# Optimization experiments

Hardware: AMD Instinct MI355X
Metric: run time of the kernel (lower is better)

The kernel has to match this reference:

```python
import jax, jax.numpy as jnp
import numpy as np

N_NODES = 100000
N_EDGES = 1600000
D_IN = 256
D_OUT = 128


def setup_inputs() -> dict:
    key = jax.random.key(0)
    k1, k2, k3, k4, k5, k6 = jax.random.split(key, 6)
    inp = {
        "input": jax.random.normal(k1, (N_NODES, D_IN), dtype=jnp.float32),
        "edge_row": jax.random.randint(k2, (N_EDGES,), 0, N_NODES),
        "edge_col": jax.random.randint(k3, (N_EDGES,), 0, N_NODES),
        "edge_val": jax.random.uniform(k4, (N_EDGES,), dtype=jnp.float32),
        "W": jax.random.normal(k5, (D_IN, D_OUT), dtype=jnp.float32) * (1.0 / np.sqrt(D_IN)),
        "b": jax.random.normal(k6, (D_OUT,), dtype=jnp.float32) * 0.01,
    }
    return inp


def reference(input, edge_row, edge_col, edge_val, W, b):
    # support = Linear(input)  -> [N, D_OUT]
    support = jnp.dot(input, W) + b
    # sparse.mm(adj, support): out[r] = sum_e val[e] * support[col[e]] for edges with row[e]==r
    msgs = edge_val[:, None] * support[edge_col]  # [E, D_OUT]
    agg = jax.ops.segment_sum(msgs, edge_row, num_segments=N_NODES)  # [N, D_OUT]
    return jnp.tanh(agg)
```

## Files before the change

kernel.cpp:

```cpp
#include <hip/hip_runtime.h>
#include <math.h>

#define N_NODES 100000
#define N_EDGES 1600000
#define D_IN 256
#define D_OUT 128

#define OFF_SUPPORT 0
#define OFF_COUNTS  51200000
#define OFF_CSREV   51600008
#define OFF_BSUMS   64400008
#define OFF_WTHI    64400416
#define OFF_WTLO    64465952

#define SCAN_CHUNK  1024
#define SCAN_BLOCKS ((N_NODES + SCAN_CHUNK - 1) / SCAN_CHUNK)

#define GB 128
#define GEMM_BLOCKS ((N_NODES + GB - 1) / GB)
#define EDGE_BLOCKS ((N_EDGES + 255) / 256)

typedef __attribute__((ext_vector_type(8))) short s8v;
typedef __attribute__((ext_vector_type(4))) float f4v;

__device__ __forceinline__ short f2bf(float x) {
  unsigned u = __float_as_uint(x);
  unsigned r = u + 0x7FFF + ((u >> 16) & 1);
  return (short)(r >> 16);
}
__device__ __forceinline__ float bf2f(short h) {
  return __uint_as_float(((unsigned)(unsigned short)h) << 16);
}

__device__ __forceinline__ void cvt8(float4 a, float4 b, s8v& h, s8v& l) {
  float f[8] = {a.x, a.y, a.z, a.w, b.x, b.y, b.z, b.w};
#pragma unroll
  for (int i = 0; i < 8; i++) {
    short hh = f2bf(f[i]);
    h[i] = hh;
    l[i] = f2bf(f[i] - bf2f(hh));
  }
}

typedef const float __attribute__((address_space(1)))* gas1f;
typedef float __attribute__((address_space(3)))* las3f;
__device__ __forceinline__ void gload_lds16(const float* g, float* l) {
  __builtin_amdgcn_global_load_lds((gas1f)g, (las3f)l, 16, 0, 0);
}

__global__ __launch_bounds__(256) void wconv_kernel(
    const float* __restrict__ W, short* __restrict__ wt_hi,
    short* __restrict__ wt_lo) {
  int idx = blockIdx.x * 256 + threadIdx.x;
  int k = idx >> 7;
  int n = idx & 127;
  float v = W[idx];
  short h = f2bf(v);
  wt_hi[n * 256 + k] = h;
  wt_lo[n * 256 + k] = f2bf(v - bf2f(h));
}

__global__ __launch_bounds__(256, 2) void gemm_kernel(
    const float* __restrict__ input, const short* __restrict__ wt_hi,
    const short* __restrict__ wt_lo, const float* __restrict__ b,
    float* __restrict__ support) {
  __shared__ float Af[4][2][32][32];
  const int gb = blockIdx.x;
  const int t = threadIdx.x;
  const int lane = t & 63;
  const int wv = t >> 6;
  const int qm = lane & 15;
  const int quad = lane >> 4;
  const int node0 = gb * GB;

  const int srow = lane >> 3;
  const int gc = (lane & 7) ^ srow;

  auto stage = [&](int kt, int buf) {
#pragma unroll
    for (int j = 0; j < 4; ++j) {
      int nd = node0 + wv * 32 + j * 8 + srow;
      if (nd > N_NODES - 1) nd = N_NODES - 1;
      gload_lds16(input + (size_t)nd * D_IN + kt * 32 + gc * 4,
                  &Af[wv][buf][j * 8][0]);
    }
  };

  stage(0, 0);
  stage(1, 1);

  f4v acc[2][8];
#pragma unroll
  for (int mt = 0; mt < 2; mt++)
#pragma unroll
    for (int nt = 0; nt < 8; nt++) acc[mt][nt] = (f4v){0.f, 0.f, 0.f, 0.f};

  const int p0 = (2 * quad) ^ (qm & 7);
  const int p1 = (2 * quad + 1) ^ (qm & 7);

#pragma unroll
  for (int kt = 0; kt < 8; ++kt) {
    const int cb = kt & 1;
    asm volatile("s_waitcnt vmcnt(4)" ::: "memory");
    float4 x00 = *(const float4*)&Af[wv][cb][qm][p0 * 4];
    float4 x01 = *(const float4*)&Af[wv][cb][qm][p1 * 4];
    float4 x10 = *(const float4*)&Af[wv][cb][qm + 16][p0 * 4];
    float4 x11 = *(const float4*)&Af[wv][cb][qm + 16][p1 * 4];
    asm volatile("s_waitcnt lgkmcnt(0)" ::: "memory");
    __builtin_amdgcn_sched_barrier(0);

    const int koff = kt * 32 + quad * 8;
    s8v bh[8], bl[8];
#pragma unroll
    for (int nt = 0; nt < 8; ++nt) {
      size_t bo = (size_t)(nt * 16 + qm) * 256 + koff;
      bh[nt] = *(const s8v*)(wt_hi + bo);
      bl[nt] = *(const s8v*)(wt_lo + bo);
    }
    __builtin_amdgcn_sched_barrier(0);
    if (kt < 6) stage(kt + 2, cb);
    __builtin_amdgcn_sched_barrier(0);

    s8v ah0, al0, ah1, al1;
    cvt8(x00, x01, ah0, al0);
    cvt8(x10, x11, ah1, al1);
#pragma unroll
    for (int nt = 0; nt < 8; ++nt) {
      acc[0][nt] = __builtin_amdgcn_mfma_f32_16x16x32_bf16(ah0, bh[nt], acc[0][nt], 0, 0, 0);
      acc[0][nt] = __builtin_amdgcn_mfma_f32_16x16x32_bf16(ah0, bl[nt], acc[0][nt], 0, 0, 0);
      acc[0][nt] = __builtin_amdgcn_mfma_f32_16x16x32_bf16(al0, bh[nt], acc[0][nt], 0, 0, 0);
      acc[1][nt] = __builtin_amdgcn_mfma_f32_16x16x32_bf16(ah1, bh[nt], acc[1][nt], 0, 0, 0);
      acc[1][nt] = __builtin_amdgcn_mfma_f32_16x16x32_bf16(ah1, bl[nt], acc[1][nt], 0, 0, 0);
      acc[1][nt] = __builtin_amdgcn_mfma_f32_16x16x32_bf16(al1, bh[nt], acc[1][nt], 0, 0, 0);
    }
  }

  float bias[8];
#pragma unroll
  for (int nt = 0; nt < 8; nt++) bias[nt] = b[nt * 16 + qm];
#pragma unroll
  for (int mt = 0; mt < 2; mt++) {
#pragma unroll
    for (int nt = 0; nt < 8; nt++) {
      int col = nt * 16 + qm;
#pragma unroll
      for (int r = 0; r < 4; r++) {
        int node = node0 + wv * 32 + mt * 16 + quad * 4 + r;
        if (node < N_NODES)
          support[(size_t)node * D_OUT + col] = acc[mt][nt][r] + bias[nt];
      }
    }
  }
}

__global__ __launch_bounds__(256) void hist_kernel(
    const int* __restrict__ erow, int* __restrict__ counts,
    int* __restrict__ pos_e) {
  int e = blockIdx.x * 256 + threadIdx.x;
  if (e < N_EDGES) pos_e[e] = atomicAdd(&counts[erow[e]], 1);
}

__global__ __launch_bounds__(256) void build_kernel(
    const int* __restrict__ erow, const int* __restrict__ ecol,
    const float* __restrict__ eval, const int* __restrict__ offsets,
    const int* __restrict__ pos_e, int2* __restrict__ csr_ev) {
  int e = blockIdx.x * 256 + threadIdx.x;
  if (e < N_EDGES) {
    int idx = offsets[erow[e]] + pos_e[e];
    csr_ev[idx] = make_int2(ecol[e], __float_as_int(eval[e]));
  }
}

__global__ __launch_bounds__(256) void scan_phase1(const int* __restrict__ counts,
                                                   int* __restrict__ bsums) {
  __shared__ int ts[256];
  int t = threadIdx.x;
  int idx0 = blockIdx.x * SCAN_CHUNK + t * 4;
  int s = 0;
#pragma unroll
  for (int i = 0; i < 4; i++)
    if (idx0 + i < N_NODES) s += counts[idx0 + i];
  ts[t] = s;
  __syncthreads();
#pragma unroll
  for (int off = 128; off > 0; off >>= 1) {
    if (t < off) ts[t] += ts[t + off];
    __syncthreads();
  }
  if (t == 0) bsums[blockIdx.x] = ts[0];
}

__global__ __launch_bounds__(128) void scan_phase2(int* __restrict__ bsums) {
  __shared__ int s[128];
  int t = threadIdx.x;
  int v = (t < SCAN_BLOCKS) ? bsums[t] : 0;
  s[t] = v;
  __syncthreads();
#pragma unroll
  for (int off = 1; off < 128; off <<= 1) {
    int x = (t >= off) ? s[t - off] : 0;
    __syncthreads();
    s[t] += x;
    __syncthreads();
  }
  if (t < SCAN_BLOCKS) bsums[t] = s[t] - v;
}

__global__ __launch_bounds__(256) void scan_phase3(int* __restrict__ counts,
                                                   const int* __restrict__ bsums) {
  __shared__ int ts[256];
  int t = threadIdx.x;
  int b = blockIdx.x;
  int idx0 = b * SCAN_CHUNK + t * 4;
  int v[4];
  int s = 0;
#pragma unroll
  for (int i = 0; i < 4; i++) {
    v[i] = (idx0 + i < N_NODES) ? counts[idx0 + i] : 0;
    s += v[i];
  }
  ts[t] = s;
  __syncthreads();
#pragma unroll
  for (int off = 1; off < 256; off <<= 1) {
    int x = (t >= off) ? ts[t - off] : 0;
    __syncthreads();
    ts[t] += x;
    __syncthreads();
  }
  int run = bsums[b] + ts[t] - s;
#pragma unroll
  for (int i = 0; i < 4; i++) {
    int idx = idx0 + i;
    if (idx < N_NODES) counts[idx] = run;
    run += v[i];
  }
  if (b == 0 && t == 0) counts[N_NODES] = N_EDGES;
}

__global__ __launch_bounds__(256) void agg_kernel(
    const int* __restrict__ offsets, const int2* __restrict__ csr_ev,
    const float* __restrict__ support, float* __restrict__ out) {
  int r = blockIdx.x * 8 + (threadIdx.x >> 5);
  int l4 = (threadIdx.x & 31) * 4;
  int beg = offsets[r];
  int end = offsets[r + 1];
  float4 acc = make_float4(0.f, 0.f, 0.f, 0.f);
  int j = beg;
  for (; j + 8 <= end; j += 8) {
    int2 e[8];
    float4 s[8];
#pragma unroll
    for (int u = 0; u < 8; u++) e[u] = csr_ev[j + u];
#pragma unroll
    for (int u = 0; u < 8; u++)
      s[u] = *(const float4*)(support + (size_t)e[u].x * D_OUT + l4);
#pragma unroll
    for (int u = 0; u < 8; u++) {
      float v = __int_as_float(e[u].y);
      acc.x = fmaf(v, s[u].x, acc.x);
      acc.y = fmaf(v, s[u].y, acc.y);
      acc.z = fmaf(v, s[u].z, acc.z);
      acc.w = fmaf(v, s[u].w, acc.w);
    }
  }
  for (; j < end; j++) {
    int2 ev = csr_ev[j];
    float4 s = *(const float4*)(support + (size_t)ev.x * D_OUT + l4);
    float v = __int_as_float(ev.y);
    acc.x = fmaf(v, s.x, acc.x);
    acc.y = fmaf(v, s.y, acc.y);
    acc.z = fmaf(v, s.z, acc.z);
    acc.w = fmaf(v, s.w, acc.w);
  }
  *(float4*)(out + (size_t)r * D_OUT + l4) =
      make_float4(tanhf(acc.x), tanhf(acc.y), tanhf(acc.z), tanhf(acc.w));
}

extern "C" void kernel_launch(void* const* d_in, const int* in_sizes, int n_in,
                              void* d_out, int out_size, void* d_ws, size_t ws_size,
                              hipStream_t stream) {
  const float* input = (const float*)d_in[0];
  const int* erow = (const int*)d_in[1];
  const int* ecol = (const int*)d_in[2];
  const float* eval = (const float*)d_in[3];
  const float* W = (const float*)d_in[4];
  const float* b = (const float*)d_in[5];
  float* out = (float*)d_out;

  char* ws = (char*)d_ws;
  float* support = (float*)(ws + OFF_SUPPORT);
  int* counts = (int*)(ws + OFF_COUNTS);
  int2* csr_ev = (int2*)(ws + OFF_CSREV);
  int* bsums = (int*)(ws + OFF_BSUMS);
  short* wt_hi = (short*)(ws + OFF_WTHI);
  short* wt_lo = (short*)(ws + OFF_WTLO);
  int* pos_e = (int*)d_out;

  hipLaunchKernelGGL(wconv_kernel, dim3((D_IN * D_OUT) / 256), dim3(256), 0,
                     stream, W, wt_hi, wt_lo);
  hipMemsetAsync(ws + OFF_COUNTS, 0, (size_t)(N_NODES + 1) * 4, stream);

  hipLaunchKernelGGL(hist_kernel, dim3(EDGE_BLOCKS), dim3(256), 0, stream,
                     erow, counts, pos_e);
  hipLaunchKernelGGL(gemm_kernel, dim3(GEMM_BLOCKS), dim3(256), 0, stream,
                     input, wt_hi, wt_lo, b, support);
  hipLaunchKernelGGL(scan_phase1, dim3(SCAN_BLOCKS), dim3(256), 0, stream,
                     counts, bsums);
  hipLaunchKernelGGL(scan_phase2, dim3(1), dim3(128), 0, stream, bsums);
  hipLaunchKernelGGL(scan_phase3, dim3(SCAN_BLOCKS), dim3(256), 0, stream,
                     counts, bsums);
  hipLaunchKernelGGL(build_kernel, dim3(EDGE_BLOCKS), dim3(256), 0, stream,
                     erow, ecol, eval, counts, pos_e, csr_ev);
  hipLaunchKernelGGL(agg_kernel, dim3(N_NODES / 8), dim3(256), 0, stream,
                     counts, csr_ev, support, out);
}
```

Measured before the change: 475.7 us.

## Fuse GEMM with histogram, fold memset into wconv, prefetch CSR edges in aggregation

Merges the edge histogram into the GEMM launch as extra blocks, so the atomic counting runs alongside the dense matmul in one grid. The counts memset moves into the weight-conversion kernel. The aggregation loop now prefetches the next 8 CSR entries while gathering the current ones, with tail lanes masked by a zero weight. The fused kernel inherits the GEMM's launch bounds and shared-memory footprint for the histogram blocks, which can limit their occupancy.

```diff
diff --git a/kernel.cpp b/kernel.cpp
--- a/kernel.cpp
+++ b/kernel.cpp
@@ -50,7 +50,7 @@
 
 __global__ __launch_bounds__(256) void wconv_kernel(
     const float* __restrict__ W, short* __restrict__ wt_hi,
-    short* __restrict__ wt_lo) {
+    short* __restrict__ wt_lo, int* __restrict__ counts) {
   int idx = blockIdx.x * 256 + threadIdx.x;
   int k = idx >> 7;
   int n = idx & 127;
@@ -58,14 +58,14 @@
   short h = f2bf(v);
   wt_hi[n * 256 + k] = h;
   wt_lo[n * 256 + k] = f2bf(v - bf2f(h));
-}
-
-__global__ __launch_bounds__(256, 2) void gemm_kernel(
-    const float* __restrict__ input, const short* __restrict__ wt_hi,
+  for (int i = idx; i < N_NODES + 1; i += 32768) counts[i] = 0;
+}
+
+__device__ __forceinline__ void gemm_body(
+    int gb, const float* __restrict__ input, const short* __restrict__ wt_hi,
     const short* __restrict__ wt_lo, const float* __restrict__ b,
     float* __restrict__ support) {
   __shared__ float Af[4][2][32][32];
-  const int gb = blockIdx.x;
   const int t = threadIdx.x;
   const int lane = t & 63;
   const int wv = t >> 6;
@@ -153,11 +153,17 @@
   }
 }
 
-__global__ __launch_bounds__(256) void hist_kernel(
-    const int* __restrict__ erow, int* __restrict__ counts,
-    int* __restrict__ pos_e) {
-  int e = blockIdx.x * 256 + threadIdx.x;
-  if (e < N_EDGES) pos_e[e] = atomicAdd(&counts[erow[e]], 1);
+__global__ __launch_bounds__(256, 2) void gemm_hist_kernel(
+    const float* __restrict__ input, const short* __restrict__ wt_hi,
+    const short* __restrict__ wt_lo, const float* __restrict__ b,
+    float* __restrict__ support, const int* __restrict__ erow,
+    int* __restrict__ counts, int* __restrict__ pos_e) {
+  if (blockIdx.x < GEMM_BLOCKS) {
+    gemm_body(blockIdx.x, input, wt_hi, wt_lo, b, support);
+  } else {
+    int e = (blockIdx.x - GEMM_BLOCKS) * 256 + threadIdx.x;
+    if (e < N_EDGES) pos_e[e] = atomicAdd(&counts[erow[e]], 1);
+  }
 }
 
 __global__ __launch_bounds__(256) void build_kernel(
@@ -246,32 +252,42 @@
   int beg = offsets[r];
   int end = offsets[r + 1];
   float4 acc = make_float4(0.f, 0.f, 0.f, 0.f);
-  int j = beg;
-  for (; j + 8 <= end; j += 8) {
-    int2 e[8];
-    float4 s[8];
-#pragma unroll
-    for (int u = 0; u < 8; u++) e[u] = csr_ev[j + u];
-#pragma unroll
-    for (int u = 0; u < 8; u++)
-      s[u] = *(const float4*)(support + (size_t)e[u].x * D_OUT + l4);
+
+  if (end > beg) {
+    int2 e[8], en[8];
 #pragma unroll
     for (int u = 0; u < 8; u++) {
-      float v = __int_as_float(e[u].y);
-      acc.x = fmaf(v, s[u].x, acc.x);
-      acc.y = fmaf(v, s[u].y, acc.y);
-      acc.z = fmaf(v, s[u].z, acc.z);
-      acc.w = fmaf(v, s[u].w, acc.w);
-    }
-  }
-  for (; j < end; j++) {
-    int2 ev = csr_ev[j];
-    float4 s = *(const float4*)(support + (size_t)ev.x * D_OUT + l4);
-    float v = __int_as_float(ev.y);
-    acc.x = fmaf(v, s.x, acc.x);
-    acc.y = fmaf(v, s.y, acc.y);
-    acc.z = fmaf(v, s.z, acc.z);
-    acc.w = fmaf(v, s.w, acc.w);
+      int idx = beg + u;
+      int c = idx < end ? idx : end - 1;
+      e[u] = csr_ev[c];
+      if (idx >= end) e[u].y = 0;
+    }
+    for (int j = beg; j < end; j += 8) {
+      int jn = j + 8;
+      if (jn < end) {
+#pragma unroll
+        for (int u = 0; u < 8; u++) {
+          int idx = jn + u;
+          int c = idx < end ? idx : end - 1;
+          en[u] = csr_ev[c];
+          if (idx >= end) en[u].y = 0;
+        }
+      }
+      float4 s[8];
+#pragma unroll
+      for (int u = 0; u < 8; u++)
+        s[u] = *(const float4*)(support + (size_t)e[u].x * D_OUT + l4);
+#pragma unroll
+      for (int u = 0; u < 8; u++) {
+        float v = __int_as_float(e[u].y);
+        acc.x = fmaf(v, s[u].x, acc.x);
+        acc.y = fmaf(v, s[u].y, acc.y);
+        acc.z = fmaf(v, s[u].z, acc.z);
+        acc.w = fmaf(v, s[u].w, acc.w);
+      }
+#pragma unroll
+      for (int u = 0; u < 8; u++) e[u] = en[u];
+    }
   }
   *(float4*)(out + (size_t)r * D_OUT + l4) =
       make_float4(tanhf(acc.x), tanhf(acc.y), tanhf(acc.z), tanhf(acc.w));
@@ -298,13 +314,11 @@
   int* pos_e = (int*)d_out;
 
   hipLaunchKernelGGL(wconv_kernel, dim3((D_IN * D_OUT) / 256), dim3(256), 0,
-                     stream, W, wt_hi, wt_lo);
-  hipMemsetAsync(ws + OFF_COUNTS, 0, (size_t)(N_NODES + 1) * 4, stream);
-
-  hipLaunchKernelGGL(hist_kernel, dim3(EDGE_BLOCKS), dim3(256), 0, stream,
+                     stream, W, wt_hi, wt_lo, counts);
+
+  hipLaunchKernelGGL(gemm_hist_kernel, dim3(GEMM_BLOCKS + EDGE_BLOCKS),
+                     dim3(256), 0, stream, input, wt_hi, wt_lo, b, support,
                      erow, counts, pos_e);
-  hipLaunchKernelGGL(gemm_kernel, dim3(GEMM_BLOCKS), dim3(256), 0, stream,
-                     input, wt_hi, wt_lo, b, support);
   hipLaunchKernelGGL(scan_phase1, dim3(SCAN_BLOCKS), dim3(256), 0, stream,
                      counts, bsums);
   hipLaunchKernelGGL(scan_phase2, dim3(1), dim3(128), 0, stream, bsums);
```

Measured after the change: 438.2 us. 7.9% less time.
